# Optimization experiments

Measured on AMD Instinct MI355X. Metric: run time of the kernel, lower is better.

Reference implementation:

```python
import jax, jax.numpy as jnp
import numpy as np

B, CH, T = 8, 512, 1024
HEADS = 8
KC = CH // HEADS  # 64
BLOCK = 256       # block_length


def setup_inputs() -> dict:
    key = jax.random.key(0)
    ks = jax.random.split(key, 10)
    s = 0.05
    x = jax.random.normal(ks[0], (B, CH, T), jnp.float32)
    c = jax.random.normal(ks[1], (B, CH, T), jnp.float32)
    attn_mask = jnp.ones((1, 1, T, T), jnp.int32)
    # 1x1 Conv1d weights are just [out, in] matrices over the channel dim.
    Wq = jax.random.normal(ks[2], (CH, CH), jnp.float32) * s
    bq = jax.random.normal(ks[3], (CH,), jnp.float32) * s
    Wk = jax.random.normal(ks[4], (CH, CH), jnp.float32) * s
    bk = jax.random.normal(ks[5], (CH,), jnp.float32) * s
    Wv = jax.random.normal(ks[6], (CH, CH), jnp.float32) * s
    bv = jax.random.normal(ks[7], (CH,), jnp.float32) * s
    Wo = jax.random.normal(ks[8], (CH, CH), jnp.float32) * s
    bo = jax.random.normal(ks[9], (CH,), jnp.float32) * s
    return {"x": x, "c": c, "attn_mask": attn_mask,
            "Wq": Wq, "bq": bq, "Wk": Wk, "bk": bk,
            "Wv": Wv, "bv": bv, "Wo": Wo, "bo": bo}


def _proj(W, b, z):
    # 1x1 Conv1d: [B,C,T] -> [B,O,T]
    return jnp.einsum('oc,bct->bot', W, z) + b[None, :, None]


def reference(x, c, attn_mask, Wq, bq, Wk, bk, Wv, bv, Wo, bo):
    q = _proj(Wq, bq, x)
    k = _proj(Wk, bk, c)
    v = _proj(Wv, bv, c)

    def split_heads(z):  # [B,C,T] -> [B,H,T,KC]
        return z.reshape(B, HEADS, KC, T).transpose(0, 1, 3, 2)

    qh, kh, vh = split_heads(q), split_heads(k), split_heads(v)

    scale = jnp.asarray(1.0 / np.sqrt(KC), qh.dtype)
    scores = jnp.einsum('bhtd,bhsd->bhts', qh * scale, kh)  # [B,H,T,T]

    r = jnp.arange(T)
    diff = jnp.abs(r[None, :] - r[:, None])  # |i - j|, [T,T]
    # proximal bias: -log(1 + |i-j|)
    scores = scores + (-jnp.log1p(diff.astype(scores.dtype)))[None, None]
    # attention mask: masked_fill(mask == 0, -1e4)
    scores = jnp.where(attn_mask == 0, jnp.asarray(-1e4, scores.dtype), scores)
    # block-length band mask: keep |i-j| <= BLOCK (triu(-BLOCK).tril(BLOCK))
    band = (diff <= BLOCK)[None, None]
    scores = jnp.where(band, scores, jnp.asarray(-1e4, scores.dtype))

    p_attn = jax.nn.softmax(scores, axis=-1)
    out = jnp.einsum('bhts,bhsd->bhtd', p_attn, vh)  # [B,H,T,KC]
    out = out.transpose(0, 1, 3, 2).reshape(B, CH, T)  # merge heads -> [B,C,T]
    return _proj(Wo, bo, out)
```

## Files before the change

### kernel.cpp

```cpp
#include <hip/hip_runtime.h>
#include <stdint.h>

typedef unsigned short u16;
typedef __attribute__((ext_vector_type(8))) __bf16 bf16x8;
typedef __attribute__((ext_vector_type(4))) float f32x4;

constexpr int B_ = 8, CH = 512, T = 1024, NH = 8, HD = 64, BAND = 256;

__device__ inline u16 f2b(float f) {
  union { float f; uint32_t u; } v; v.f = f;
  uint32_t r = (v.u + 0x7fffu + ((v.u >> 16) & 1u)) >> 16;
  return (u16)r;
}

__device__ inline f32x4 mfma16(bf16x8 a, bf16x8 b, f32x4 c) {
  return __builtin_amdgcn_mfma_f32_16x16x32_bf16(a, b, c, 0, 0, 0);
}

__device__ __forceinline__ void gld16(const void* g, void* l) {
  __builtin_amdgcn_global_load_lds((__attribute__((address_space(1))) void*)(g),
                                   (__attribute__((address_space(3))) void*)(l),
                                   16, 0, 0);
}

__device__ __forceinline__ float exp2_hw(float x) { return __builtin_amdgcn_exp2f(x); }

__global__ __launch_bounds__(256) void prep(const float* __restrict__ x, const float* __restrict__ c,
                                            const float* __restrict__ wq, const float* __restrict__ wk,
                                            const float* __restrict__ wv, const float* __restrict__ wo,
                                            u16* __restrict__ xT, u16* __restrict__ cT, u16* __restrict__ Wb) {
  int z = blockIdx.z, tid = threadIdx.x;
  if (z == 16) {
    int wb = blockIdx.y * 16 + blockIdx.x;
    int w = wb >> 5;
    const float* src = (w == 0) ? wq : (w == 1) ? wk : (w == 2) ? wv : wo;
    int base = (wb & 31) * 8192;
#pragma unroll
    for (int i = 0; i < 4; i++) {
      int e = base + i * 2048 + tid * 8;
      f32x4 a = *(const f32x4*)(src + e);
      f32x4 b = *(const f32x4*)(src + e + 4);
      union { u16 h[8]; bf16x8 v; } r;
      r.h[0] = f2b(a[0]); r.h[1] = f2b(a[1]); r.h[2] = f2b(a[2]); r.h[3] = f2b(a[3]);
      r.h[4] = f2b(b[0]); r.h[5] = f2b(b[1]); r.h[6] = f2b(b[2]); r.h[7] = f2b(b[3]);
      *(bf16x8*)(Wb + (w << 18) + e) = r.v;
    }
    return;
  }
  __shared__ float tile[64][65];
  int b = z & 7;
  const float* src = (z < 8) ? x : c;
  u16* dst = (z < 8) ? xT : cT;
  int t0 = blockIdx.x * 64, c0 = blockIdx.y * 64;
  int t4 = (tid & 15) * 4, chb = tid >> 4;
#pragma unroll
  for (int p = 0; p < 4; p++) {
    int ch = chb + p * 16;
    f32x4 v = *(const f32x4*)(src + (long)(b * CH + c0 + ch) * T + t0 + t4);
#pragma unroll
    for (int j = 0; j < 4; j++) tile[t4 + j][ch] = v[j];
  }
  __syncthreads();
  int o = tid & 7, trr = tid >> 3;
#pragma unroll
  for (int p = 0; p < 2; p++) {
    int tr = trr + p * 32;
    union { u16 h[8]; bf16x8 v; } r;
#pragma unroll
    for (int j = 0; j < 8; j++) r.h[j] = f2b(tile[tr][o * 8 + j]);
    *(bf16x8*)(dst + (long)(b * T + t0 + tr) * CH + c0 + o * 8) = r.v;
  }
}

template <int TN, typename OT>
__device__ __forceinline__ void gemm_core(const u16* __restrict__ Ab, int lda,
                                          const u16* __restrict__ Bb, int ldb,
                                          OT* __restrict__ Cb, int ldc,
                                          const float* __restrict__ bi, bool brow,
                                          int m0, int n0, int K, u16* smA, u16* smB) {
  int t = threadIdx.x, lane = t & 63, wave = t >> 6;
  int cl = lane & 15, quad = lane >> 4;
  int wm = wave >> 1, wn = wave & 1;
  int rr = t >> 3, gs = t & 7;
  constexpr int NW = TN / 32;
  f32x4 acc[4][NW] = {};
  for (int k0 = 0; k0 < K; k0 += 64) {
    __syncthreads();
#pragma unroll
    for (int j = 0; j < 4; j++) {
      int R = j * 32 + rr;
      int gc = (gs ^ (R & 7)) << 3;
      gld16(Ab + (long)(m0 + R) * lda + k0 + gc, (char*)smA + j * 4096 + wave * 1024);
      if (j < TN / 32)
        gld16(Bb + (long)(n0 + R) * ldb + k0 + gc, (char*)smB + j * 4096 + wave * 1024);
    }
    __syncthreads();
#pragma unroll
    for (int ks = 0; ks < 2; ks++) {
      int g2 = ((ks << 2) | quad) ^ (cl & 7);
      bf16x8 af[4], bb[NW];
#pragma unroll
      for (int i = 0; i < 4; i++)
        af[i] = *(const bf16x8*)&smA[(wm * 64 + i * 16 + cl) * 64 + g2 * 8];
#pragma unroll
      for (int i = 0; i < NW; i++)
        bb[i] = *(const bf16x8*)&smB[(wn * (TN / 2) + i * 16 + cl) * 64 + g2 * 8];
#pragma unroll
      for (int mi = 0; mi < 4; mi++)
#pragma unroll
        for (int ni = 0; ni < NW; ni++)
          acc[mi][ni] = mfma16(af[mi], bb[ni], acc[mi][ni]);
    }
  }
#pragma unroll
  for (int mi = 0; mi < 4; mi++) {
    int row = m0 + wm * 64 + mi * 16 + quad * 4;
#pragma unroll
    for (int ni = 0; ni < NW; ni++) {
      int col = n0 + wn * (TN / 2) + ni * 16 + cl;
#pragma unroll
      for (int r = 0; r < 4; r++) {
        float v = acc[mi][ni][r] + (brow ? bi[row + r] : bi[col]);
        if constexpr (sizeof(OT) == 2) Cb[(long)(row + r) * ldc + col] = f2b(v);
        else Cb[(long)(row + r) * ldc + col] = v;
      }
    }
  }
}

__global__ __launch_bounds__(256, 3) void gemm_qkv(const u16* __restrict__ xT, const u16* __restrict__ cT,
                                                   const u16* __restrict__ Wb,
                                                   u16* __restrict__ Qb, u16* __restrict__ Kb, u16* __restrict__ Vb,
                                                   const float* __restrict__ bq, const float* __restrict__ bk,
                                                   const float* __restrict__ bv) {
  __shared__ u16 smA[128 * 64], smB[128 * 64];
  const long TCH = (long)T * CH;
  int z = blockIdx.z, sec = z >> 3, zz = z & 7, bx = blockIdx.x;
  const u16 *Ab, *Bb; u16* Cb; const float* bi;
  int m0, n0, ldc; bool brow;
  if (sec == 0) {
    Ab = xT + zz * TCH; Bb = Wb;           Cb = Qb + zz * TCH;        bi = bq;
    m0 = (bx >> 2) * 128; n0 = (bx & 3) * 128; ldc = CH; brow = false;
  } else if (sec == 1) {
    Ab = cT + zz * TCH; Bb = Wb + 262144;  Cb = Kb + zz * TCH;        bi = bk;
    m0 = (bx >> 2) * 128; n0 = (bx & 3) * 128; ldc = CH; brow = false;
  } else {
    Ab = Wb + 2 * 262144; Bb = cT + zz * TCH; Cb = Vb + zz * (long)CH * T; bi = bv;
    m0 = (bx & 3) * 128; n0 = (bx >> 2) * 128; ldc = T; brow = true;
  }
  gemm_core<128, u16>(Ab, CH, Bb, CH, Cb, ldc, bi, brow, m0, n0, CH, smA, smB);
}

__global__ __launch_bounds__(256, 4) void gemm_o(const u16* __restrict__ Wo, const u16* __restrict__ AO,
                                                 float* __restrict__ out, const float* __restrict__ bo) {
  __shared__ u16 smA[128 * 64], smB[64 * 64];
  int z = blockIdx.z;
  gemm_core<64, float>(Wo, CH, AO + z * (long)T * CH, CH, out + z * (long)CH * T, T,
                       bo, true, blockIdx.y * 128, blockIdx.x * 64, CH, smA, smB);
}

__global__ __launch_bounds__(256, 4) void attn(const u16* __restrict__ Q, const u16* __restrict__ Kt,
                                               const u16* __restrict__ V, u16* __restrict__ AO) {
  __shared__ u16 sK[2][64 * 64];
  __shared__ u16 sV[2][64 * 64];
  __shared__ u16 sP[4][16 * 64];
  int lane = threadIdx.x & 63, wave = threadIdx.x >> 6;
  int cl = lane & 15, quad = lane >> 4;
  int bx = blockIdx.x;
  int xcd = bx & 7, ii = bx >> 3;
  int bh = xcd * 8 + (ii & 7);
  int qt = ii >> 3;
  int b = bh >> 3, h = bh & 7;
  int tq0 = qt * 64;
  int tqw = tq0 + wave * 16;
  const u16* qb = Q + ((long)(b * T + tqw + cl) * CH) + h * HD;
  bf16x8 qf0 = *(const bf16x8*)(qb + quad * 8);
  bf16x8 qf1 = *(const bf16x8*)(qb + 32 + quad * 8);
  f32x4 acc[4] = {};
  float lr[4] = {0.f, 0.f, 0.f, 0.f};
  float fir[4];
#pragma unroll
  for (int r = 0; r < 4; r++) fir[r] = (float)(tqw + quad * 4 + r);
  int lo = tq0 - BAND; if (lo < 0) lo = 0;
  int hi = tq0 + 64 + BAND; if (hi > T) hi = T;
  int nt = (hi - lo) >> 6;

  int rl = lane >> 3, cg = lane & 7;
  const u16* ksrc = Kt + (long)b * T * CH + h * HD;
  const u16* vsrc = V + ((long)(b * CH + h * HD) * T);

#define STAGE(buf, j0)                                                          \
  {                                                                             \
    _Pragma("unroll")                                                           \
    for (int i = 0; i < 2; i++) {                                               \
      int r = wave * 16 + i * 8 + rl;                                           \
      int s = ((r >> 5) << 5) + ((r >> 4) & 1) + ((r & 15) << 1);               \
      gld16(ksrc + (long)(j0 + s) * CH + ((cg ^ (r & 7)) << 3),                 \
            (char*)&sK[buf][(wave * 16 + i * 8) * 64]);                         \
      gld16(vsrc + (long)r * T + (j0) + ((cg ^ (r & 7)) << 3),                  \
            (char*)&sV[buf][(wave * 16 + i * 8) * 64]);                         \
    }                                                                           \
  }

  STAGE(0, lo)
  constexpr float C2 = 0.125f * 1.4426950408889634f;
  for (int it = 0; it < nt; it++) {
    int cur = it & 1;
    int j0 = lo + it * 64;
    __syncthreads();
    if (it + 1 < nt) STAGE(1 - cur, j0 + 64)
    f32x4 sg[2][2];
#pragma unroll
    for (int p = 0; p < 2; p++)
#pragma unroll
      for (int sub = 0; sub < 2; sub++) {
        const u16* kr = &sK[cur][(p * 32 + sub * 16 + cl) * 64];
        bf16x8 k0 = *(const bf16x8*)&kr[((quad ^ (cl & 7)) << 3)];
        bf16x8 k1 = *(const bf16x8*)&kr[(((4 | quad) ^ (cl & 7)) << 3)];
        f32x4 z = {0.f, 0.f, 0.f, 0.f};
        sg[p][sub] = mfma16(qf1, k1, mfma16(qf0, k0, z));
      }
#pragma unroll
    for (int p = 0; p < 2; p++) {
      float jb = (float)(j0 + p * 32 + 2 * cl);
#pragma unroll
      for (int r = 0; r < 4; r++) {
        float de = fabsf(fir[r] - jb);
        float dd = fabsf(fir[r] - jb - 1.f);
        float pe = exp2_hw(sg[p][0][r] * C2) * __builtin_amdgcn_rcpf(1.f + de);
        float po = exp2_hw(sg[p][1][r] * C2) * __builtin_amdgcn_rcpf(1.f + dd);
        pe = (de <= 256.f) ? pe : 0.f;
        po = (dd <= 256.f) ? po : 0.f;
        lr[r] += pe + po;
        uint32_t pk;
        asm("v_cvt_pk_bf16_f32 %0, %1, %2" : "=v"(pk) : "v"(pe), "v"(po));
        int R = (quad << 2) | r;
        *(uint32_t*)&sP[wave][(R << 6) + ((((p << 2) | (cl >> 2)) ^ (R & 7)) << 3) +
                              ((cl & 3) << 1)] = pk;
      }
    }
#pragma unroll
    for (int ks = 0; ks < 2; ks++) {
      bf16x8 pf = *(bf16x8*)&sP[wave][(cl << 6) + ((((ks << 2) | quad) ^ (cl & 7)) << 3)];
#pragma unroll
      for (int dg = 0; dg < 4; dg++) {
        bf16x8 vf = *(const bf16x8*)&sV[cur][(dg * 16 + cl) * 64 +
                                             ((((ks << 2) | quad) ^ (cl & 7)) << 3)];
        acc[dg] = mfma16(pf, vf, acc[dg]);
      }
    }
  }
#undef STAGE
  float inv[4];
#pragma unroll
  for (int r = 0; r < 4; r++) {
    float s = lr[r];
    s += __shfl_xor(s, 1); s += __shfl_xor(s, 2);
    s += __shfl_xor(s, 4); s += __shfl_xor(s, 8);
    inv[r] = __builtin_amdgcn_rcpf(s);
  }
#pragma unroll
  for (int dg = 0; dg < 4; dg++)
#pragma unroll
    for (int r = 0; r < 4; r++)
      AO[((long)(b * T + tqw + quad * 4 + r) * CH) + h * HD + dg * 16 + cl] = f2b(acc[dg][r] * inv[r]);
}

extern "C" void kernel_launch(void* const* d_in, const int* in_sizes, int n_in,
                              void* d_out, int out_size, void* d_ws, size_t ws_size,
                              hipStream_t stream) {
  const float* x  = (const float*)d_in[0];
  const float* c  = (const float*)d_in[1];
  const float* Wq = (const float*)d_in[3];
  const float* bq = (const float*)d_in[4];
  const float* Wk = (const float*)d_in[5];
  const float* bk = (const float*)d_in[6];
  const float* Wv = (const float*)d_in[7];
  const float* bv = (const float*)d_in[8];
  const float* Wo = (const float*)d_in[9];
  const float* bo = (const float*)d_in[10];
  float* out = (float*)d_out;

  const long NT = (long)B_ * T * CH;
  u16* Wb = (u16*)d_ws;
  u16* xT = Wb + 4 * 262144;
  u16* cT = xT + NT;
  u16* Qb = cT + NT;
  u16* Kb = Qb + NT;
  u16* Vb = Kb + NT;
  u16* AO = xT;

  prep<<<dim3(16, 8, 17), dim3(256), 0, stream>>>(x, c, Wq, Wk, Wv, Wo, xT, cT, Wb);
  gemm_qkv<<<dim3(32, 1, 24), dim3(256), 0, stream>>>(xT, cT, Wb, Qb, Kb, Vb, bq, bk, bv);
  attn<<<dim3(1024), dim3(256), 0, stream>>>(Qb, Kb, Vb, AO);
  gemm_o<<<dim3(16, 4, 8), dim3(256), 0, stream>>>(Wb + 3 * 262144, AO, out, bo);
}
```

Measured before the change: 151.9 us.

## Flatten grids for XCD-aware batch mapping, pair-pack epilogue stores, share reciprocal

Launches prep, gemm_qkv and gemm_o on 1D grids. The low 3 bits of the block id pick the batch, so blocks that share a batch likely land on the same XCD and reuse its L2. Epilogues in the GEMMs and in attention swap values between neighbouring lanes and write packed pairs (bf16x2 or float2) instead of scalar stores. The attention bias computation replaces two reciprocals with one reciprocal of the product plus two multiplies. These changes add shuffles and may lose a little precision in the bias.

Result: slower. 155.3 us (+2.3%).

```diff
diff --git a/kernel.cpp b/kernel.cpp
--- a/kernel.cpp
+++ b/kernel.cpp
@@ -4,6 +4,7 @@
 typedef unsigned short u16;
 typedef __attribute__((ext_vector_type(8))) __bf16 bf16x8;
 typedef __attribute__((ext_vector_type(4))) float f32x4;
+typedef __attribute__((ext_vector_type(2))) float f32x2;
 
 constexpr int B_ = 8, CH = 512, T = 1024, NH = 8, HD = 64, BAND = 256;
 
@@ -29,9 +30,9 @@
                                             const float* __restrict__ wq, const float* __restrict__ wk,
                                             const float* __restrict__ wv, const float* __restrict__ wo,
                                             u16* __restrict__ xT, u16* __restrict__ cT, u16* __restrict__ Wb) {
-  int z = blockIdx.z, tid = threadIdx.x;
-  if (z == 16) {
-    int wb = blockIdx.y * 16 + blockIdx.x;
+  int bid = blockIdx.x, tid = threadIdx.x;
+  if (bid >= 2048) {
+    int wb = bid - 2048;
     int w = wb >> 5;
     const float* src = (w == 0) ? wq : (w == 1) ? wk : (w == 2) ? wv : wo;
     int base = (wb & 31) * 8192;
@@ -48,10 +49,11 @@
     return;
   }
   __shared__ float tile[64][65];
-  int b = z & 7;
-  const float* src = (z < 8) ? x : c;
-  u16* dst = (z < 8) ? xT : cT;
-  int t0 = blockIdx.x * 64, c0 = blockIdx.y * 64;
+  int b = bid & 7, k = bid >> 3;
+  const float* src = (k < 128) ? x : c;
+  u16* dst = (k < 128) ? xT : cT;
+  int rem = k & 127;
+  int t0 = (rem & 15) * 64, c0 = (rem >> 4) * 64;
   int t4 = (tid & 15) * 4, chb = tid >> 4;
 #pragma unroll
   for (int p = 0; p < 4; p++) {
@@ -112,17 +114,33 @@
           acc[mi][ni] = mfma16(af[mi], bb[ni], acc[mi][ni]);
     }
   }
+  bool ev = ((cl & 1) == 0);
 #pragma unroll
   for (int mi = 0; mi < 4; mi++) {
     int row = m0 + wm * 64 + mi * 16 + quad * 4;
 #pragma unroll
     for (int ni = 0; ni < NW; ni++) {
       int col = n0 + wn * (TN / 2) + ni * 16 + cl;
-#pragma unroll
-      for (int r = 0; r < 4; r++) {
-        float v = acc[mi][ni][r] + (brow ? bi[row + r] : bi[col]);
-        if constexpr (sizeof(OT) == 2) Cb[(long)(row + r) * ldc + col] = f2b(v);
-        else Cb[(long)(row + r) * ldc + col] = v;
+      float v0 = acc[mi][ni][0] + (brow ? bi[row + 0] : bi[col]);
+      float v1 = acc[mi][ni][1] + (brow ? bi[row + 1] : bi[col]);
+      float v2 = acc[mi][ni][2] + (brow ? bi[row + 2] : bi[col]);
+      float v3 = acc[mi][ni][3] + (brow ? bi[row + 3] : bi[col]);
+      float p0 = __shfl_xor(v0, 1), p1 = __shfl_xor(v1, 1);
+      float p2 = __shfl_xor(v2, 1), p3 = __shfl_xor(v3, 1);
+      float lo0 = ev ? v0 : p1, hi0 = ev ? p0 : v1;
+      float lo1 = ev ? v2 : p3, hi1 = ev ? p2 : v3;
+      int r0 = ev ? 0 : 1, r1 = ev ? 2 : 3;
+      long a0 = (long)(row + r0) * ldc + (col & ~1);
+      long a1 = (long)(row + r1) * ldc + (col & ~1);
+      if constexpr (sizeof(OT) == 2) {
+        uint32_t w0, w1;
+        asm("v_cvt_pk_bf16_f32 %0, %1, %2" : "=v"(w0) : "v"(lo0), "v"(hi0));
+        asm("v_cvt_pk_bf16_f32 %0, %1, %2" : "=v"(w1) : "v"(lo1), "v"(hi1));
+        *(uint32_t*)&Cb[a0] = w0;
+        *(uint32_t*)&Cb[a1] = w1;
+      } else {
+        *(f32x2*)&Cb[a0] = (f32x2){lo0, hi0};
+        *(f32x2*)&Cb[a1] = (f32x2){lo1, hi1};
       }
     }
   }
@@ -135,7 +153,8 @@
                                                    const float* __restrict__ bv) {
   __shared__ u16 smA[128 * 64], smB[128 * 64];
   const long TCH = (long)T * CH;
-  int z = blockIdx.z, sec = z >> 3, zz = z & 7, bx = blockIdx.x;
+  int bid = blockIdx.x;
+  int zz = bid & 7, r = bid >> 3, sec = r >> 5, bx = r & 31;
   const u16 *Ab, *Bb; u16* Cb; const float* bi;
   int m0, n0, ldc; bool brow;
   if (sec == 0) {
@@ -154,9 +173,10 @@
 __global__ __launch_bounds__(256, 4) void gemm_o(const u16* __restrict__ Wo, const u16* __restrict__ AO,
                                                  float* __restrict__ out, const float* __restrict__ bo) {
   __shared__ u16 smA[128 * 64], smB[64 * 64];
-  int z = blockIdx.z;
+  int bid = blockIdx.x;
+  int z = bid & 7, r = bid >> 3;
   gemm_core<64, float>(Wo, CH, AO + z * (long)T * CH, CH, out + z * (long)CH * T, T,
-                       bo, true, blockIdx.y * 128, blockIdx.x * 64, CH, smA, smB);
+                       bo, true, (r >> 4) * 128, (r & 15) * 64, CH, smA, smB);
 }
 
 __global__ __launch_bounds__(256, 4) void attn(const u16* __restrict__ Q, const u16* __restrict__ Kt,
@@ -227,8 +247,10 @@
       for (int r = 0; r < 4; r++) {
         float de = fabsf(fir[r] - jb);
         float dd = fabsf(fir[r] - jb - 1.f);
-        float pe = exp2_hw(sg[p][0][r] * C2) * __builtin_amdgcn_rcpf(1.f + de);
-        float po = exp2_hw(sg[p][1][r] * C2) * __builtin_amdgcn_rcpf(1.f + dd);
+        float we = 1.f + de, wd = 1.f + dd;
+        float rb = __builtin_amdgcn_rcpf(we * wd);
+        float pe = exp2_hw(sg[p][0][r] * C2) * (wd * rb);
+        float po = exp2_hw(sg[p][1][r] * C2) * (we * rb);
         pe = (de <= 256.f) ? pe : 0.f;
         po = (dd <= 256.f) ? po : 0.f;
         lr[r] += pe + po;
@@ -259,11 +281,23 @@
     s += __shfl_xor(s, 4); s += __shfl_xor(s, 8);
     inv[r] = __builtin_amdgcn_rcpf(s);
   }
-#pragma unroll
-  for (int dg = 0; dg < 4; dg++)
-#pragma unroll
-    for (int r = 0; r < 4; r++)
-      AO[((long)(b * T + tqw + quad * 4 + r) * CH) + h * HD + dg * 16 + cl] = f2b(acc[dg][r] * inv[r]);
+  bool ev = ((cl & 1) == 0);
+#pragma unroll
+  for (int dg = 0; dg < 4; dg++) {
+    float v0 = acc[dg][0] * inv[0], v1 = acc[dg][1] * inv[1];
+    float v2 = acc[dg][2] * inv[2], v3 = acc[dg][3] * inv[3];
+    float p0 = __shfl_xor(v0, 1), p1 = __shfl_xor(v1, 1);
+    float p2 = __shfl_xor(v2, 1), p3 = __shfl_xor(v3, 1);
+    float lo0 = ev ? v0 : p1, hi0 = ev ? p0 : v1;
+    float lo1 = ev ? v2 : p3, hi1 = ev ? p2 : v3;
+    int r0 = ev ? 0 : 1, r1 = ev ? 2 : 3;
+    uint32_t w0, w1;
+    asm("v_cvt_pk_bf16_f32 %0, %1, %2" : "=v"(w0) : "v"(lo0), "v"(hi0));
+    asm("v_cvt_pk_bf16_f32 %0, %1, %2" : "=v"(w1) : "v"(lo1), "v"(hi1));
+    int cb = h * HD + ((dg * 16 + cl) & ~1);
+    *(uint32_t*)&AO[(long)(b * T + tqw + quad * 4 + r0) * CH + cb] = w0;
+    *(uint32_t*)&AO[(long)(b * T + tqw + quad * 4 + r1) * CH + cb] = w1;
+  }
 }
 
 extern "C" void kernel_launch(void* const* d_in, const int* in_sizes, int n_in,
@@ -290,8 +324,8 @@
   u16* Vb = Kb + NT;
   u16* AO = xT;
 
-  prep<<<dim3(16, 8, 17), dim3(256), 0, stream>>>(x, c, Wq, Wk, Wv, Wo, xT, cT, Wb);
-  gemm_qkv<<<dim3(32, 1, 24), dim3(256), 0, stream>>>(xT, cT, Wb, Qb, Kb, Vb, bq, bk, bv);
+  prep<<<dim3(2176), dim3(256), 0, stream>>>(x, c, Wq, Wk, Wv, Wo, xT, cT, Wb);
+  gemm_qkv<<<dim3(768), dim3(256), 0, stream>>>(xT, cT, Wb, Qb, Kb, Vb, bq, bk, bv);
   attn<<<dim3(1024), dim3(256), 0, stream>>>(Qb, Kb, Vb, AO);
-  gemm_o<<<dim3(16, 4, 8), dim3(256), 0, stream>>>(Wb + 3 * 262144, AO, out, bo);
-}
+  gemm_o<<<dim3(512), dim3(256), 0, stream>>>(Wb + 3 * 262144, AO, out, bo);
+}
```

## Flatten grids with XCD-aware block mapping, pack bf16 conversions, specialize band clamp

Applied to the files above, without the earlier changes.

Converts prep, gemm_qkv and gemm_o launches to 1D grids whose block index places the batch in the low bits, so blocks of the same batch spread across XCDs in a different pattern. Replaces scalar software bf16 rounding with packed v_cvt_pk_bf16_f32 in prep. In attention, one reciprocal of the product of the two proximal-bias weights replaces two reciprocals, and the band clamp is skipped for key tiles fully inside the band. These target cache locality, conversion ALU work and transcendental count, at the cost of slightly different rounding of the bias weights and more code.

Result: slower. 156.2 us (+2.9%).

```diff
diff --git a/kernel.cpp b/kernel.cpp
--- a/kernel.cpp
+++ b/kernel.cpp
@@ -29,9 +29,9 @@
                                             const float* __restrict__ wq, const float* __restrict__ wk,
                                             const float* __restrict__ wv, const float* __restrict__ wo,
                                             u16* __restrict__ xT, u16* __restrict__ cT, u16* __restrict__ Wb) {
-  int z = blockIdx.z, tid = threadIdx.x;
-  if (z == 16) {
-    int wb = blockIdx.y * 16 + blockIdx.x;
+  int bid = blockIdx.x, tid = threadIdx.x;
+  if (bid >= 2048) {
+    int wb = bid - 2048;
     int w = wb >> 5;
     const float* src = (w == 0) ? wq : (w == 1) ? wk : (w == 2) ? wv : wo;
     int base = (wb & 31) * 8192;
@@ -40,18 +40,21 @@
       int e = base + i * 2048 + tid * 8;
       f32x4 a = *(const f32x4*)(src + e);
       f32x4 b = *(const f32x4*)(src + e + 4);
-      union { u16 h[8]; bf16x8 v; } r;
-      r.h[0] = f2b(a[0]); r.h[1] = f2b(a[1]); r.h[2] = f2b(a[2]); r.h[3] = f2b(a[3]);
-      r.h[4] = f2b(b[0]); r.h[5] = f2b(b[1]); r.h[6] = f2b(b[2]); r.h[7] = f2b(b[3]);
+      union { uint32_t w[4]; bf16x8 v; } r;
+      asm("v_cvt_pk_bf16_f32 %0, %1, %2" : "=v"(r.w[0]) : "v"(a[0]), "v"(a[1]));
+      asm("v_cvt_pk_bf16_f32 %0, %1, %2" : "=v"(r.w[1]) : "v"(a[2]), "v"(a[3]));
+      asm("v_cvt_pk_bf16_f32 %0, %1, %2" : "=v"(r.w[2]) : "v"(b[0]), "v"(b[1]));
+      asm("v_cvt_pk_bf16_f32 %0, %1, %2" : "=v"(r.w[3]) : "v"(b[2]), "v"(b[3]));
       *(bf16x8*)(Wb + (w << 18) + e) = r.v;
     }
     return;
   }
   __shared__ float tile[64][65];
-  int b = z & 7;
-  const float* src = (z < 8) ? x : c;
-  u16* dst = (z < 8) ? xT : cT;
-  int t0 = blockIdx.x * 64, c0 = blockIdx.y * 64;
+  int b = bid & 7, k = bid >> 3;
+  const float* src = (k < 128) ? x : c;
+  u16* dst = (k < 128) ? xT : cT;
+  int rem = k & 127;
+  int t0 = (rem & 15) * 64, c0 = (rem >> 4) * 64;
   int t4 = (tid & 15) * 4, chb = tid >> 4;
 #pragma unroll
   for (int p = 0; p < 4; p++) {
@@ -65,9 +68,12 @@
 #pragma unroll
   for (int p = 0; p < 2; p++) {
     int tr = trr + p * 32;
-    union { u16 h[8]; bf16x8 v; } r;
-#pragma unroll
-    for (int j = 0; j < 8; j++) r.h[j] = f2b(tile[tr][o * 8 + j]);
+    union { uint32_t w[4]; bf16x8 v; } r;
+#pragma unroll
+    for (int j = 0; j < 4; j++) {
+      float e0 = tile[tr][o * 8 + 2 * j], e1 = tile[tr][o * 8 + 2 * j + 1];
+      asm("v_cvt_pk_bf16_f32 %0, %1, %2" : "=v"(r.w[j]) : "v"(e0), "v"(e1));
+    }
     *(bf16x8*)(dst + (long)(b * T + t0 + tr) * CH + c0 + o * 8) = r.v;
   }
 }
@@ -135,7 +141,8 @@
                                                    const float* __restrict__ bv) {
   __shared__ u16 smA[128 * 64], smB[128 * 64];
   const long TCH = (long)T * CH;
-  int z = blockIdx.z, sec = z >> 3, zz = z & 7, bx = blockIdx.x;
+  int bid = blockIdx.x;
+  int zz = bid & 7, r = bid >> 3, sec = r >> 5, bx = r & 31;
   const u16 *Ab, *Bb; u16* Cb; const float* bi;
   int m0, n0, ldc; bool brow;
   if (sec == 0) {
@@ -154,9 +161,10 @@
 __global__ __launch_bounds__(256, 4) void gemm_o(const u16* __restrict__ Wo, const u16* __restrict__ AO,
                                                  float* __restrict__ out, const float* __restrict__ bo) {
   __shared__ u16 smA[128 * 64], smB[64 * 64];
-  int z = blockIdx.z;
+  int bid = blockIdx.x;
+  int z = bid & 7, r = bid >> 3;
   gemm_core<64, float>(Wo, CH, AO + z * (long)T * CH, CH, out + z * (long)CH * T, T,
-                       bo, true, blockIdx.y * 128, blockIdx.x * 64, CH, smA, smB);
+                       bo, true, (r >> 4) * 128, (r & 15) * 64, CH, smA, smB);
 }
 
 __global__ __launch_bounds__(256, 4) void attn(const u16* __restrict__ Q, const u16* __restrict__ Kt,
@@ -202,6 +210,32 @@
     }                                                                           \
   }
 
+#define SOFTMAX(CLAMP)                                                          \
+  _Pragma("unroll")                                                             \
+  for (int p = 0; p < 2; p++) {                                                 \
+    float jb = (float)(j0 + p * 32 + 2 * cl);                                   \
+    _Pragma("unroll")                                                           \
+    for (int r = 0; r < 4; r++) {                                               \
+      float tdiff = fir[r] - jb;                                                \
+      float de = fabsf(tdiff);                                                  \
+      float dd = fabsf(tdiff - 1.f);                                            \
+      float we = 1.f + de, wd = 1.f + dd;                                       \
+      float rb = __builtin_amdgcn_rcpf(we * wd);                                \
+      float pe = exp2_hw(sg[p][0][r] * C2) * (wd * rb);                         \
+      float po = exp2_hw(sg[p][1][r] * C2) * (we * rb);                         \
+      if (CLAMP) {                                                              \
+        pe = (de <= 256.f) ? pe : 0.f;                                          \
+        po = (dd <= 256.f) ? po : 0.f;                                          \
+      }                                                                         \
+      lr[r] += pe + po;                                                         \
+      uint32_t pk;                                                              \
+      asm("v_cvt_pk_bf16_f32 %0, %1, %2" : "=v"(pk) : "v"(pe), "v"(po));        \
+      int R = (quad << 2) | r;                                                  \
+      *(uint32_t*)&sP[wave][(R << 6) + ((((p << 2) | (cl >> 2)) ^ (R & 7)) << 3) + \
+                            ((cl & 3) << 1)] = pk;                              \
+    }                                                                           \
+  }
+
   STAGE(0, lo)
   constexpr float C2 = 0.125f * 1.4426950408889634f;
   for (int it = 0; it < nt; it++) {
@@ -220,25 +254,8 @@
         f32x4 z = {0.f, 0.f, 0.f, 0.f};
         sg[p][sub] = mfma16(qf1, k1, mfma16(qf0, k0, z));
       }
-#pragma unroll
-    for (int p = 0; p < 2; p++) {
-      float jb = (float)(j0 + p * 32 + 2 * cl);
-#pragma unroll
-      for (int r = 0; r < 4; r++) {
-        float de = fabsf(fir[r] - jb);
-        float dd = fabsf(fir[r] - jb - 1.f);
-        float pe = exp2_hw(sg[p][0][r] * C2) * __builtin_amdgcn_rcpf(1.f + de);
-        float po = exp2_hw(sg[p][1][r] * C2) * __builtin_amdgcn_rcpf(1.f + dd);
-        pe = (de <= 256.f) ? pe : 0.f;
-        po = (dd <= 256.f) ? po : 0.f;
-        lr[r] += pe + po;
-        uint32_t pk;
-        asm("v_cvt_pk_bf16_f32 %0, %1, %2" : "=v"(pk) : "v"(pe), "v"(po));
-        int R = (quad << 2) | r;
-        *(uint32_t*)&sP[wave][(R << 6) + ((((p << 2) | (cl >> 2)) ^ (R & 7)) << 3) +
-                              ((cl & 3) << 1)] = pk;
-      }
-    }
+    int dt = j0 - tq0;
+    if (dt < -192 || dt > 192) { SOFTMAX(true) } else { SOFTMAX(false) }
 #pragma unroll
     for (int ks = 0; ks < 2; ks++) {
       bf16x8 pf = *(bf16x8*)&sP[wave][(cl << 6) + ((((ks << 2) | quad) ^ (cl & 7)) << 3)];
@@ -251,6 +268,7 @@
     }
   }
 #undef STAGE
+#undef SOFTMAX
   float inv[4];
 #pragma unroll
   for (int r = 0; r < 4; r++) {
@@ -290,8 +308,8 @@
   u16* Vb = Kb + NT;
   u16* AO = xT;
 
-  prep<<<dim3(16, 8, 17), dim3(256), 0, stream>>>(x, c, Wq, Wk, Wv, Wo, xT, cT, Wb);
-  gemm_qkv<<<dim3(32, 1, 24), dim3(256), 0, stream>>>(xT, cT, Wb, Qb, Kb, Vb, bq, bk, bv);
+  prep<<<dim3(2176), dim3(256), 0, stream>>>(x, c, Wq, Wk, Wv, Wo, xT, cT, Wb);
+  gemm_qkv<<<dim3(768), dim3(256), 0, stream>>>(xT, cT, Wb, Qb, Kb, Vb, bq, bk, bv);
   attn<<<dim3(1024), dim3(256), 0, stream>>>(Qb, Kb, Vb, AO);
-  gemm_o<<<dim3(16, 4, 8), dim3(256), 0, stream>>>(Wb + 3 * 262144, AO, out, bo);
-}
+  gemm_o<<<dim3(512), dim3(256), 0, stream>>>(Wb + 3 * 262144, AO, out, bo);
+}
```
